# Performance work log

Measured on AMD Instinct MI355X. Metric: run time of the kernel, lower is better.

Reference implementation:

```python
import jax, jax.numpy as jnp
import numpy as np

B, N, F_IN, H, E = 8, 10000, 128, 128, 160000


def setup_inputs() -> dict:
    key = jax.random.key(0)
    ks = jax.random.split(key, 6)
    x = jax.random.normal(ks[0], (B, N, F_IN), dtype=jnp.float32)
    edge_index = jax.random.randint(ks[1], (2, E), 0, N, dtype=jnp.int64)
    # GCNConv params (glorot-ish scale), LayerNorm affine params
    W1 = jax.random.normal(ks[2], (F_IN, H), dtype=jnp.float32) / np.sqrt(F_IN)
    b1 = jnp.zeros((H,), dtype=jnp.float32)
    W2 = jax.random.normal(ks[3], (H, H), dtype=jnp.float32) / np.sqrt(H)
    b2 = jnp.zeros((H,), dtype=jnp.float32)
    ln_w = jnp.ones((H,), dtype=jnp.float32)
    ln_b = jnp.zeros((H,), dtype=jnp.float32)
    return {"x": x, "edge_index": edge_index, "W1": W1, "b1": b1,
            "W2": W2, "b2": b2, "ln_w": ln_w, "ln_b": ln_b}


def reference(x, edge_index, W1, b1, W2, b2, ln_w, ln_b):
    # x: [B, N, F]; edge_index: [2, E] shared across batch (tiled per graph
    # in the original via node offsets -> equivalent to vmapping over batch).
    n = x.shape[1]
    loops = jnp.arange(n, dtype=edge_index.dtype)
    src = jnp.concatenate([edge_index[0], loops])  # add self-loops (GCNConv default)
    dst = jnp.concatenate([edge_index[1], loops])
    # symmetric degree normalization: deg over targets with self-loops
    deg = jax.ops.segment_sum(jnp.ones(dst.shape[0], dtype=x.dtype), dst, num_segments=n)
    dinv = jnp.where(deg > 0, jax.lax.rsqrt(deg), 0.0)
    w_e = dinv[src] * dinv[dst]  # [E+N] per-edge norm

    def gcn_agg(h):  # h: [B, N, H] -> gather, scale, scatter-add
        msg = h[:, src, :] * w_e[None, :, None]  # [B, E+N, H]
        return jax.vmap(lambda m: jax.ops.segment_sum(m, dst, num_segments=n))(msg)

    h1 = jax.nn.relu(gcn_agg(x @ W1) + b1)
    h2 = gcn_agg(h1 @ W2) + b2
    # LayerNorm over last dim (eps=1e-5, torch default)
    mu = jnp.mean(h2, axis=-1, keepdims=True)
    var = jnp.mean(jnp.square(h2 - mu), axis=-1, keepdims=True)
    out = (h2 - mu) * jax.lax.rsqrt(var + 1e-5) * ln_w + ln_b
    return out  # [B, N, H]
```

## Files before the change

kernel.cpp:

```cpp
#include <hip/hip_runtime.h>
#include <hip/hip_bf16.h>

#define NNODES 10000
#define NB 8
#define NF 128
#define NE 160000

typedef __attribute__((ext_vector_type(8))) short  short8;
typedef __attribute__((ext_vector_type(8))) unsigned short ushort8;
typedef __attribute__((ext_vector_type(4))) float  f32x4;

__device__ __forceinline__ unsigned short f2b(float f) {
    union { float f; unsigned u; } v; v.f = f;
    unsigned r = v.u + 0x7FFF + ((v.u >> 16) & 1);
    return (unsigned short)(r >> 16);
}
__device__ __forceinline__ float b2f(unsigned short h) {
    union { unsigned u; float f; } v; v.u = ((unsigned)h) << 16;
    return v.f;
}
__device__ __forceinline__ float b2f_lo(unsigned u) {
    union { unsigned u; float f; } v; v.u = u << 16; return v.f;
}
__device__ __forceinline__ float b2f_hi(unsigned u) {
    union { unsigned u; float f; } v; v.u = u & 0xffff0000u; return v.f;
}


__global__ void k_zero(int* __restrict__ cnt, int* __restrict__ fill) {
    int i = blockIdx.x * blockDim.x + threadIdx.x;
    if (i < NNODES) { cnt[i] = 0; fill[i] = 0; }
}

__global__ void k_count(const int* __restrict__ ei, int* __restrict__ cnt) {
    int e = blockIdx.x * blockDim.x + threadIdx.x;
    if (e < NE) atomicAdd(&cnt[ei[NE + e]], 1);
}

__global__ void k_dinv(const int* __restrict__ cnt, float* __restrict__ dinv) {
    int i = blockIdx.x * blockDim.x + threadIdx.x;
    if (i < NNODES) dinv[i] = rsqrtf((float)(cnt[i] + 1));
}

__global__ void k_scan(const int* __restrict__ cnt, int* __restrict__ row_ptr) {
    __shared__ int part[1024];
    int t = threadIdx.x;
    const int CH = (NNODES + 1023) / 1024;
    int lo = t * CH, hi = min(lo + CH, NNODES);
    int s = 0;
    for (int i = lo; i < hi; i++) s += cnt[i];
    part[t] = s;
    __syncthreads();
    for (int off = 1; off < 1024; off <<= 1) {
        int v = (t >= off) ? part[t - off] : 0;
        __syncthreads();
        part[t] += v;
        __syncthreads();
    }
    int base = part[t] - s;
    for (int i = lo; i < hi; i++) { row_ptr[i] = base; base += cnt[i]; }
    if (t == 1023) row_ptr[NNODES] = part[1023];
}

__global__ void k_scatter(const int* __restrict__ ei, const int* __restrict__ row_ptr,
                          int* __restrict__ fill, const float* __restrict__ dinv,
                          int* __restrict__ col, float* __restrict__ wgt) {
    int e = blockIdx.x * blockDim.x + threadIdx.x;
    if (e >= NE) return;
    int s = ei[e];
    int d = ei[NE + e];
    int pos = row_ptr[d] + atomicAdd(&fill[d], 1);
    col[pos] = s;
    wgt[pos] = dinv[s] * dinv[d];
}

__global__ void k_wt(const float* __restrict__ W, unsigned short* __restrict__ Wt) {
    int id = blockIdx.x * 256 + threadIdx.x;
    int n = id >> 7, k = id & 127;
    Wt[(size_t)n * 128 + k] = f2b(W[(size_t)k * 128 + n]);
}

template <bool ABF16>
__global__ __launch_bounds__(256) void k_mm_mfma(const void* __restrict__ Ap,
                                                 const unsigned short* __restrict__ Wt,
                                                 unsigned short* __restrict__ Cn) {
    __shared__ unsigned short wlds[128 * 136];
    const int t = threadIdx.x;
    {
        const int r = t >> 1, h = t & 1;
        const ushort8* src = (const ushort8*)(Wt + r * 128 + h * 64);
        #pragma unroll
        for (int i = 0; i < 8; i++)
            *(ushort8*)(wlds + r * 136 + h * 64 + i * 8) = src[i];
    }
    __syncthreads();

    const int wid = t >> 6, lane = t & 63;
    const int quad = lane >> 4, l16 = lane & 15;
    const int m0 = blockIdx.x * 64 + (wid & 1) * 32;
    const int nb = (wid >> 1) * 64;
    const int kq = quad * 8;

    f32x4 acc[2][4] = {};

    #pragma unroll
    for (int ks = 0; ks < 128; ks += 32) {
        short8 bf[2];
        #pragma unroll
        for (int mi = 0; mi < 2; mi++) {
            const size_t row = (size_t)(m0 + mi * 16 + l16);
            if constexpr (ABF16) {
                bf[mi] = *(const short8*)((const unsigned short*)Ap + row * 128 + ks + kq);
            } else {
                const float* p = (const float*)Ap + row * 128 + ks + kq;
                float4 u0 = *(const float4*)p;
                float4 u1 = *(const float4*)(p + 4);
                short8 v;
                v[0] = (short)f2b(u0.x); v[1] = (short)f2b(u0.y);
                v[2] = (short)f2b(u0.z); v[3] = (short)f2b(u0.w);
                v[4] = (short)f2b(u1.x); v[5] = (short)f2b(u1.y);
                v[6] = (short)f2b(u1.z); v[7] = (short)f2b(u1.w);
                bf[mi] = v;
            }
        }
        short8 af[4];
        #pragma unroll
        for (int ni = 0; ni < 4; ni++)
            af[ni] = *(const short8*)(wlds + (nb + ni * 16 + l16) * 136 + ks + kq);
        #pragma unroll
        for (int mi = 0; mi < 2; mi++)
            #pragma unroll
            for (int ni = 0; ni < 4; ni++)
                acc[mi][ni] = __builtin_amdgcn_mfma_f32_16x16x32_bf16(
                    af[ni], bf[mi], acc[mi][ni], 0, 0, 0);
    }

    __syncthreads();
    {
        const int rbase = (wid & 1) * 32;
        #pragma unroll
        for (int mi = 0; mi < 2; mi++) {
            int rr = rbase + mi * 16 + l16;
            #pragma unroll
            for (int ni = 0; ni < 4; ni++) {
                ushort4 o;
                o.x = f2b(acc[mi][ni][0]); o.y = f2b(acc[mi][ni][1]);
                o.z = f2b(acc[mi][ni][2]); o.w = f2b(acc[mi][ni][3]);
                *(ushort4*)(wlds + rr * 136 + nb + ni * 16 + quad * 4) = o;
            }
        }
    }
    __syncthreads();
    {
        const int r = t >> 2, seg = t & 3;
        int gm = blockIdx.x * 64 + r;
        int b = gm / NNODES;
        int n = gm - b * NNODES;
        unsigned short* dst = Cn + ((size_t)n * NB + b) * 128 + seg * 32;
        const unsigned short* srow = wlds + r * 136 + seg * 32;
        #pragma unroll
        for (int i = 0; i < 4; i++)
            *(ushort8*)(dst + i * 8) = *(const ushort8*)(srow + i * 8);
    }
}


__global__ __launch_bounds__(256) void k_agg_relu(const unsigned int* __restrict__ hNu,
                                                  const float* __restrict__ bias,
                                                  const int* __restrict__ row_ptr,
                                                  const int* __restrict__ col,
                                                  const float* __restrict__ wgt,
                                                  const float* __restrict__ dinv,
                                                  unsigned int* __restrict__ h1u) {
    const int t = threadIdx.x;
    const int b = blockIdx.x & 7;
    const int g = blockIdx.x >> 3;
    const int wid = __builtin_amdgcn_readfirstlane(t >> 6);
    const int lane = t & 63;
    const int n = g * 4 + wid;

    const unsigned int* base = hNu + (size_t)b * 64 + lane;
    float di = dinv[n];
    float wself = di * di;
    unsigned int u = base[(size_t)n * 512];
    float a0 = b2f_lo(u) * wself;
    float a1 = b2f_hi(u) * wself;

    int e = row_ptr[n], e1 = row_ptr[n + 1];
    for (; e + 4 <= e1; e += 4) {
        int s0 = col[e], s1 = col[e + 1], s2 = col[e + 2], s3 = col[e + 3];
        float w0 = wgt[e], w1 = wgt[e + 1], w2 = wgt[e + 2], w3 = wgt[e + 3];
        unsigned int u0 = base[(size_t)s0 * 512];
        unsigned int u1 = base[(size_t)s1 * 512];
        unsigned int u2 = base[(size_t)s2 * 512];
        unsigned int u3 = base[(size_t)s3 * 512];
        a0 = fmaf(b2f_lo(u0), w0, a0); a1 = fmaf(b2f_hi(u0), w0, a1);
        a0 = fmaf(b2f_lo(u1), w1, a0); a1 = fmaf(b2f_hi(u1), w1, a1);
        a0 = fmaf(b2f_lo(u2), w2, a0); a1 = fmaf(b2f_hi(u2), w2, a1);
        a0 = fmaf(b2f_lo(u3), w3, a0); a1 = fmaf(b2f_hi(u3), w3, a1);
    }
    for (; e < e1; ++e) {
        int s = col[e]; float w = wgt[e];
        unsigned int uu = base[(size_t)s * 512];
        a0 = fmaf(b2f_lo(uu), w, a0); a1 = fmaf(b2f_hi(uu), w, a1);
    }
    a0 = fmaxf(a0 + bias[lane * 2], 0.f);
    a1 = fmaxf(a1 + bias[lane * 2 + 1], 0.f);
    unsigned int o = (unsigned int)f2b(a0) | ((unsigned int)f2b(a1) << 16);
    __builtin_nontemporal_store(o, &h1u[((size_t)b * NNODES + n) * 64 + lane]);
}

__global__ __launch_bounds__(256) void k_agg_ln(const unsigned int* __restrict__ hNu,
                                                const float* __restrict__ bias,
                                                const int* __restrict__ row_ptr,
                                                const int* __restrict__ col,
                                                const float* __restrict__ wgt,
                                                const float* __restrict__ dinv,
                                                const float* __restrict__ ln_w,
                                                const float* __restrict__ ln_b,
                                                float* __restrict__ out) {
    const int t = threadIdx.x;
    const int b = blockIdx.x & 7;
    const int g = blockIdx.x >> 3;
    const int wid = __builtin_amdgcn_readfirstlane(t >> 6);
    const int lane = t & 63;
    const int n = g * 4 + wid;

    const unsigned int* base = hNu + (size_t)b * 64 + lane;
    float di = dinv[n];
    float wself = di * di;
    unsigned int u = base[(size_t)n * 512];
    float a0 = b2f_lo(u) * wself;
    float a1 = b2f_hi(u) * wself;

    int e = row_ptr[n], e1 = row_ptr[n + 1];
    for (; e + 4 <= e1; e += 4) {
        int s0 = col[e], s1 = col[e + 1], s2 = col[e + 2], s3 = col[e + 3];
        float w0 = wgt[e], w1 = wgt[e + 1], w2 = wgt[e + 2], w3 = wgt[e + 3];
        unsigned int u0 = base[(size_t)s0 * 512];
        unsigned int u1 = base[(size_t)s1 * 512];
        unsigned int u2 = base[(size_t)s2 * 512];
        unsigned int u3 = base[(size_t)s3 * 512];
        a0 = fmaf(b2f_lo(u0), w0, a0); a1 = fmaf(b2f_hi(u0), w0, a1);
        a0 = fmaf(b2f_lo(u1), w1, a0); a1 = fmaf(b2f_hi(u1), w1, a1);
        a0 = fmaf(b2f_lo(u2), w2, a0); a1 = fmaf(b2f_hi(u2), w2, a1);
        a0 = fmaf(b2f_lo(u3), w3, a0); a1 = fmaf(b2f_hi(u3), w3, a1);
    }
    for (; e < e1; ++e) {
        int s = col[e]; float w = wgt[e];
        unsigned int uu = base[(size_t)s * 512];
        a0 = fmaf(b2f_lo(uu), w, a0); a1 = fmaf(b2f_hi(uu), w, a1);
    }
    a0 += bias[lane * 2];
    a1 += bias[lane * 2 + 1];

    float s1 = a0 + a1;
    float s2 = a0 * a0 + a1 * a1;
    #pragma unroll
    for (int m = 1; m < 64; m <<= 1) {
        s1 += __shfl_xor(s1, m);
        s2 += __shfl_xor(s2, m);
    }
    float mu = s1 * (1.f / NF);
    float var = s2 * (1.f / NF) - mu * mu;
    float rs = rsqrtf(var + 1e-5f);

    float o0 = (a0 - mu) * rs * ln_w[lane * 2] + ln_b[lane * 2];
    float o1 = (a1 - mu) * rs * ln_w[lane * 2 + 1] + ln_b[lane * 2 + 1];
    float* dst = out + ((size_t)b * NNODES + n) * 128 + lane * 2;
    __builtin_nontemporal_store(o0, dst);
    __builtin_nontemporal_store(o1, dst + 1);
}


extern "C" void kernel_launch(void* const* d_in, const int* in_sizes, int n_in,
                              void* d_out, int out_size, void* d_ws, size_t ws_size,
                              hipStream_t stream) {
    const float* x    = (const float*)d_in[0];
    const int*   ei   = (const int*)d_in[1];
    const float* W1   = (const float*)d_in[2];
    const float* b1   = (const float*)d_in[3];
    const float* W2   = (const float*)d_in[4];
    const float* b2   = (const float*)d_in[5];
    const float* ln_w = (const float*)d_in[6];
    const float* ln_b = (const float*)d_in[7];
    float* out = (float*)d_out;

    char* ws = (char*)d_ws;
    int*            cnt     = (int*)(ws + 0);
    int*            fill    = (int*)(ws + 40192);
    int*            row_ptr = (int*)(ws + 80384);
    float*          dinv    = (float*)(ws + 120832);
    int*            col     = (int*)(ws + 161024);
    float*          wgt     = (float*)(ws + 801024);
    unsigned short* hA16    = (unsigned short*)(ws + 1441024);
    unsigned short* h1b     = (unsigned short*)(ws + 21921024);
    unsigned short* Wt1     = (unsigned short*)cnt;
    unsigned short* Wt2     = (unsigned short*)fill;

    k_zero   <<<(NNODES + 255) / 256, 256, 0, stream>>>(cnt, fill);
    k_count  <<<(NE + 255) / 256, 256, 0, stream>>>(ei, cnt);
    k_dinv   <<<(NNODES + 255) / 256, 256, 0, stream>>>(cnt, dinv);
    k_scan   <<<1, 1024, 0, stream>>>(cnt, row_ptr);
    k_scatter<<<(NE + 255) / 256, 256, 0, stream>>>(ei, row_ptr, fill, dinv, col, wgt);

    k_wt<<<64, 256, 0, stream>>>(W1, Wt1);
    k_wt<<<64, 256, 0, stream>>>(W2, Wt2);

    k_mm_mfma<false><<<(NB * NNODES) / 64, 256, 0, stream>>>(x, Wt1, hA16);
    k_agg_relu<<<(NNODES / 4) * NB, 256, 0, stream>>>((const unsigned int*)hA16, b1,
                                                      row_ptr, col, wgt, dinv,
                                                      (unsigned int*)h1b);

    k_mm_mfma<true><<<(NB * NNODES) / 64, 256, 0, stream>>>(h1b, Wt2, hA16);
    k_agg_ln<<<(NNODES / 4) * NB, 256, 0, stream>>>((const unsigned int*)hA16, b2,
                                                    row_ptr, col, wgt, dinv,
                                                    ln_w, ln_b, out);
}
```

Baseline: 240.0 us.

## Pack edges into uint2, fuse setup kernels, enlarge GEMM tiles, deepen gather unroll

Interleaves the CSR column index and edge weight into a single uint2 array so each aggregated edge needs one load instead of two. The dinv kernel is folded into the scan, and the two weight transposes share one launch, cutting launch count. The MFMA GEMM now covers 128 rows per block instead of 64, and bf16 conversion uses packed pair conversions. The aggregation loops unroll by 8 to keep more gathers in flight, at the cost of more registers.

```diff
diff --git a/kernel.cpp b/kernel.cpp
--- a/kernel.cpp
+++ b/kernel.cpp
@@ -15,9 +15,10 @@
     unsigned r = v.u + 0x7FFF + ((v.u >> 16) & 1);
     return (unsigned short)(r >> 16);
 }
-__device__ __forceinline__ float b2f(unsigned short h) {
-    union { unsigned u; float f; } v; v.u = ((unsigned)h) << 16;
-    return v.f;
+__device__ __forceinline__ unsigned int f2b2(float a, float b) {
+    union { __hip_bfloat162 h; unsigned int u; } v;
+    v.h = __float22bfloat162_rn(make_float2(a, b));
+    return v.u;
 }
 __device__ __forceinline__ float b2f_lo(unsigned u) {
     union { unsigned u; float f; } v; v.u = u << 16; return v.f;
@@ -29,7 +30,8 @@
 
 __global__ void k_zero(int* __restrict__ cnt, int* __restrict__ fill) {
     int i = blockIdx.x * blockDim.x + threadIdx.x;
-    if (i < NNODES) { cnt[i] = 0; fill[i] = 0; }
+    if (i < NNODES) cnt[i] = 0;
+    else if (i < 2 * NNODES) fill[i - NNODES] = 0;
 }
 
 __global__ void k_count(const int* __restrict__ ei, int* __restrict__ cnt) {
@@ -37,18 +39,18 @@
     if (e < NE) atomicAdd(&cnt[ei[NE + e]], 1);
 }
 
-__global__ void k_dinv(const int* __restrict__ cnt, float* __restrict__ dinv) {
-    int i = blockIdx.x * blockDim.x + threadIdx.x;
-    if (i < NNODES) dinv[i] = rsqrtf((float)(cnt[i] + 1));
-}
-
-__global__ void k_scan(const int* __restrict__ cnt, int* __restrict__ row_ptr) {
+__global__ void k_scan(const int* __restrict__ cnt, int* __restrict__ row_ptr,
+                       float* __restrict__ dinv) {
     __shared__ int part[1024];
     int t = threadIdx.x;
     const int CH = (NNODES + 1023) / 1024;
     int lo = t * CH, hi = min(lo + CH, NNODES);
     int s = 0;
-    for (int i = lo; i < hi; i++) s += cnt[i];
+    for (int i = lo; i < hi; i++) {
+        int c = cnt[i];
+        dinv[i] = rsqrtf((float)(c + 1));
+        s += c;
+    }
     part[t] = s;
     __syncthreads();
     for (int off = 1; off < 1024; off <<= 1) {
@@ -64,18 +66,21 @@
 
 __global__ void k_scatter(const int* __restrict__ ei, const int* __restrict__ row_ptr,
                           int* __restrict__ fill, const float* __restrict__ dinv,
-                          int* __restrict__ col, float* __restrict__ wgt) {
+                          uint2* __restrict__ edge) {
     int e = blockIdx.x * blockDim.x + threadIdx.x;
     if (e >= NE) return;
     int s = ei[e];
     int d = ei[NE + e];
     int pos = row_ptr[d] + atomicAdd(&fill[d], 1);
-    col[pos] = s;
-    wgt[pos] = dinv[s] * dinv[d];
-}
-
-__global__ void k_wt(const float* __restrict__ W, unsigned short* __restrict__ Wt) {
-    int id = blockIdx.x * 256 + threadIdx.x;
+    edge[pos] = make_uint2((unsigned)s, __float_as_uint(dinv[s] * dinv[d]));
+}
+
+__global__ void k_wt2(const float* __restrict__ W1, unsigned short* __restrict__ Wt1,
+                      const float* __restrict__ W2, unsigned short* __restrict__ Wt2) {
+    int bid = blockIdx.x;
+    const float* W = (bid < 64) ? W1 : W2;
+    unsigned short* Wt = (bid < 64) ? Wt1 : Wt2;
+    int id = (bid & 63) * 256 + threadIdx.x;
     int n = id >> 7, k = id & 127;
     Wt[(size_t)n * 128 + k] = f2b(W[(size_t)k * 128 + n]);
 }
@@ -97,17 +102,17 @@
 
     const int wid = t >> 6, lane = t & 63;
     const int quad = lane >> 4, l16 = lane & 15;
-    const int m0 = blockIdx.x * 64 + (wid & 1) * 32;
+    const int m0 = blockIdx.x * 128 + (wid & 1) * 64;
     const int nb = (wid >> 1) * 64;
     const int kq = quad * 8;
 
-    f32x4 acc[2][4] = {};
+    f32x4 acc[4][4] = {};
 
     #pragma unroll
     for (int ks = 0; ks < 128; ks += 32) {
-        short8 bf[2];
-        #pragma unroll
-        for (int mi = 0; mi < 2; mi++) {
+        short8 bf[4];
+        #pragma unroll
+        for (int mi = 0; mi < 4; mi++) {
             const size_t row = (size_t)(m0 + mi * 16 + l16);
             if constexpr (ABF16) {
                 bf[mi] = *(const short8*)((const unsigned short*)Ap + row * 128 + ks + kq);
@@ -115,12 +120,10 @@
                 const float* p = (const float*)Ap + row * 128 + ks + kq;
                 float4 u0 = *(const float4*)p;
                 float4 u1 = *(const float4*)(p + 4);
-                short8 v;
-                v[0] = (short)f2b(u0.x); v[1] = (short)f2b(u0.y);
-                v[2] = (short)f2b(u0.z); v[3] = (short)f2b(u0.w);
-                v[4] = (short)f2b(u1.x); v[5] = (short)f2b(u1.y);
-                v[6] = (short)f2b(u1.z); v[7] = (short)f2b(u1.w);
-                bf[mi] = v;
+                union { uint4 u4; short8 s8; } cv;
+                cv.u4.x = f2b2(u0.x, u0.y); cv.u4.y = f2b2(u0.z, u0.w);
+                cv.u4.z = f2b2(u1.x, u1.y); cv.u4.w = f2b2(u1.z, u1.w);
+                bf[mi] = cv.s8;
             }
         }
         short8 af[4];
@@ -128,7 +131,7 @@
         for (int ni = 0; ni < 4; ni++)
             af[ni] = *(const short8*)(wlds + (nb + ni * 16 + l16) * 136 + ks + kq);
         #pragma unroll
-        for (int mi = 0; mi < 2; mi++)
+        for (int mi = 0; mi < 4; mi++)
             #pragma unroll
             for (int ni = 0; ni < 4; ni++)
                 acc[mi][ni] = __builtin_amdgcn_mfma_f32_16x16x32_bf16(
@@ -137,29 +140,29 @@
 
     __syncthreads();
     {
-        const int rbase = (wid & 1) * 32;
-        #pragma unroll
-        for (int mi = 0; mi < 2; mi++) {
+        const int rbase = (wid & 1) * 64;
+        #pragma unroll
+        for (int mi = 0; mi < 4; mi++) {
             int rr = rbase + mi * 16 + l16;
             #pragma unroll
             for (int ni = 0; ni < 4; ni++) {
-                ushort4 o;
-                o.x = f2b(acc[mi][ni][0]); o.y = f2b(acc[mi][ni][1]);
-                o.z = f2b(acc[mi][ni][2]); o.w = f2b(acc[mi][ni][3]);
-                *(ushort4*)(wlds + rr * 136 + nb + ni * 16 + quad * 4) = o;
+                uint2 p;
+                p.x = f2b2(acc[mi][ni][0], acc[mi][ni][1]);
+                p.y = f2b2(acc[mi][ni][2], acc[mi][ni][3]);
+                *(uint2*)(wlds + rr * 136 + nb + ni * 16 + quad * 4) = p;
             }
         }
     }
     __syncthreads();
     {
-        const int r = t >> 2, seg = t & 3;
-        int gm = blockIdx.x * 64 + r;
+        const int r = t >> 1, h = t & 1;
+        int gm = blockIdx.x * 128 + r;
         int b = gm / NNODES;
         int n = gm - b * NNODES;
-        unsigned short* dst = Cn + ((size_t)n * NB + b) * 128 + seg * 32;
-        const unsigned short* srow = wlds + r * 136 + seg * 32;
-        #pragma unroll
-        for (int i = 0; i < 4; i++)
+        unsigned short* dst = Cn + ((size_t)n * NB + b) * 128 + h * 64;
+        const unsigned short* srow = wlds + r * 136 + h * 64;
+        #pragma unroll
+        for (int i = 0; i < 8; i++)
             *(ushort8*)(dst + i * 8) = *(const ushort8*)(srow + i * 8);
     }
 }
@@ -168,8 +171,7 @@
 __global__ __launch_bounds__(256) void k_agg_relu(const unsigned int* __restrict__ hNu,
                                                   const float* __restrict__ bias,
                                                   const int* __restrict__ row_ptr,
-                                                  const int* __restrict__ col,
-                                                  const float* __restrict__ wgt,
+                                                  const uint2* __restrict__ edge,
                                                   const float* __restrict__ dinv,
                                                   unsigned int* __restrict__ h1u) {
     const int t = threadIdx.x;
@@ -187,34 +189,50 @@
     float a1 = b2f_hi(u) * wself;
 
     int e = row_ptr[n], e1 = row_ptr[n + 1];
+    for (; e + 8 <= e1; e += 8) {
+        uint2 E[8];
+        #pragma unroll
+        for (int j = 0; j < 8; j++) E[j] = edge[e + j];
+        unsigned int U[8];
+        #pragma unroll
+        for (int j = 0; j < 8; j++) U[j] = base[(size_t)E[j].x * 512];
+        #pragma unroll
+        for (int j = 0; j < 8; j++) {
+            float w = __uint_as_float(E[j].y);
+            a0 = fmaf(b2f_lo(U[j]), w, a0);
+            a1 = fmaf(b2f_hi(U[j]), w, a1);
+        }
+    }
     for (; e + 4 <= e1; e += 4) {
-        int s0 = col[e], s1 = col[e + 1], s2 = col[e + 2], s3 = col[e + 3];
-        float w0 = wgt[e], w1 = wgt[e + 1], w2 = wgt[e + 2], w3 = wgt[e + 3];
-        unsigned int u0 = base[(size_t)s0 * 512];
-        unsigned int u1 = base[(size_t)s1 * 512];
-        unsigned int u2 = base[(size_t)s2 * 512];
-        unsigned int u3 = base[(size_t)s3 * 512];
-        a0 = fmaf(b2f_lo(u0), w0, a0); a1 = fmaf(b2f_hi(u0), w0, a1);
-        a0 = fmaf(b2f_lo(u1), w1, a0); a1 = fmaf(b2f_hi(u1), w1, a1);
-        a0 = fmaf(b2f_lo(u2), w2, a0); a1 = fmaf(b2f_hi(u2), w2, a1);
-        a0 = fmaf(b2f_lo(u3), w3, a0); a1 = fmaf(b2f_hi(u3), w3, a1);
+        uint2 E[4];
+        #pragma unroll
+        for (int j = 0; j < 4; j++) E[j] = edge[e + j];
+        unsigned int U[4];
+        #pragma unroll
+        for (int j = 0; j < 4; j++) U[j] = base[(size_t)E[j].x * 512];
+        #pragma unroll
+        for (int j = 0; j < 4; j++) {
+            float w = __uint_as_float(E[j].y);
+            a0 = fmaf(b2f_lo(U[j]), w, a0);
+            a1 = fmaf(b2f_hi(U[j]), w, a1);
+        }
     }
     for (; e < e1; ++e) {
-        int s = col[e]; float w = wgt[e];
-        unsigned int uu = base[(size_t)s * 512];
-        a0 = fmaf(b2f_lo(uu), w, a0); a1 = fmaf(b2f_hi(uu), w, a1);
+        uint2 E = edge[e];
+        float w = __uint_as_float(E.y);
+        unsigned int uu = base[(size_t)E.x * 512];
+        a0 = fmaf(b2f_lo(uu), w, a0);
+        a1 = fmaf(b2f_hi(uu), w, a1);
     }
     a0 = fmaxf(a0 + bias[lane * 2], 0.f);
     a1 = fmaxf(a1 + bias[lane * 2 + 1], 0.f);
-    unsigned int o = (unsigned int)f2b(a0) | ((unsigned int)f2b(a1) << 16);
-    __builtin_nontemporal_store(o, &h1u[((size_t)b * NNODES + n) * 64 + lane]);
+    __builtin_nontemporal_store(f2b2(a0, a1), &h1u[((size_t)b * NNODES + n) * 64 + lane]);
 }
 
 __global__ __launch_bounds__(256) void k_agg_ln(const unsigned int* __restrict__ hNu,
                                                 const float* __restrict__ bias,
                                                 const int* __restrict__ row_ptr,
-                                                const int* __restrict__ col,
-                                                const float* __restrict__ wgt,
+                                                const uint2* __restrict__ edge,
                                                 const float* __restrict__ dinv,
                                                 const float* __restrict__ ln_w,
                                                 const float* __restrict__ ln_b,
@@ -234,22 +252,40 @@
     float a1 = b2f_hi(u) * wself;
 
     int e = row_ptr[n], e1 = row_ptr[n + 1];
+    for (; e + 8 <= e1; e += 8) {
+        uint2 E[8];
+        #pragma unroll
+        for (int j = 0; j < 8; j++) E[j] = edge[e + j];
+        unsigned int U[8];
+        #pragma unroll
+        for (int j = 0; j < 8; j++) U[j] = base[(size_t)E[j].x * 512];
+        #pragma unroll
+        for (int j = 0; j < 8; j++) {
+            float w = __uint_as_float(E[j].y);
+            a0 = fmaf(b2f_lo(U[j]), w, a0);
+            a1 = fmaf(b2f_hi(U[j]), w, a1);
+        }
+    }
     for (; e + 4 <= e1; e += 4) {
-        int s0 = col[e], s1 = col[e + 1], s2 = col[e + 2], s3 = col[e + 3];
-        float w0 = wgt[e], w1 = wgt[e + 1], w2 = wgt[e + 2], w3 = wgt[e + 3];
-        unsigned int u0 = base[(size_t)s0 * 512];
-        unsigned int u1 = base[(size_t)s1 * 512];
-        unsigned int u2 = base[(size_t)s2 * 512];
-        unsigned int u3 = base[(size_t)s3 * 512];
-        a0 = fmaf(b2f_lo(u0), w0, a0); a1 = fmaf(b2f_hi(u0), w0, a1);
-        a0 = fmaf(b2f_lo(u1), w1, a0); a1 = fmaf(b2f_hi(u1), w1, a1);
-        a0 = fmaf(b2f_lo(u2), w2, a0); a1 = fmaf(b2f_hi(u2), w2, a1);
-        a0 = fmaf(b2f_lo(u3), w3, a0); a1 = fmaf(b2f_hi(u3), w3, a1);
+        uint2 E[4];
+        #pragma unroll
+        for (int j = 0; j < 4; j++) E[j] = edge[e + j];
+        unsigned int U[4];
+        #pragma unroll
+        for (int j = 0; j < 4; j++) U[j] = base[(size_t)E[j].x * 512];
+        #pragma unroll
+        for (int j = 0; j < 4; j++) {
+            float w = __uint_as_float(E[j].y);
+            a0 = fmaf(b2f_lo(U[j]), w, a0);
+            a1 = fmaf(b2f_hi(U[j]), w, a1);
+        }
     }
     for (; e < e1; ++e) {
-        int s = col[e]; float w = wgt[e];
-        unsigned int uu = base[(size_t)s * 512];
-        a0 = fmaf(b2f_lo(uu), w, a0); a1 = fmaf(b2f_hi(uu), w, a1);
+        uint2 E = edge[e];
+        float w = __uint_as_float(E.y);
+        unsigned int uu = base[(size_t)E.x * 512];
+        a0 = fmaf(b2f_lo(uu), w, a0);
+        a1 = fmaf(b2f_hi(uu), w, a1);
     }
     a0 += bias[lane * 2];
     a1 += bias[lane * 2 + 1];
@@ -291,29 +327,25 @@
     int*            fill    = (int*)(ws + 40192);
     int*            row_ptr = (int*)(ws + 80384);
     float*          dinv    = (float*)(ws + 120832);
-    int*            col     = (int*)(ws + 161024);
-    float*          wgt     = (float*)(ws + 801024);
+    uint2*          edge    = (uint2*)(ws + 161024);
     unsigned short* hA16    = (unsigned short*)(ws + 1441024);
     unsigned short* h1b     = (unsigned short*)(ws + 21921024);
     unsigned short* Wt1     = (unsigned short*)cnt;
     unsigned short* Wt2     = (unsigned short*)fill;
 
-    k_zero   <<<(NNODES + 255) / 256, 256, 0, stream>>>(cnt, fill);
+    k_zero   <<<(2 * NNODES + 255) / 256, 256, 0, stream>>>(cnt, fill);
     k_count  <<<(NE + 255) / 256, 256, 0, stream>>>(ei, cnt);
-    k_dinv   <<<(NNODES + 255) / 256, 256, 0, stream>>>(cnt, dinv);
-    k_scan   <<<1, 1024, 0, stream>>>(cnt, row_ptr);
-    k_scatter<<<(NE + 255) / 256, 256, 0, stream>>>(ei, row_ptr, fill, dinv, col, wgt);
-
-    k_wt<<<64, 256, 0, stream>>>(W1, Wt1);
-    k_wt<<<64, 256, 0, stream>>>(W2, Wt2);
-
-    k_mm_mfma<false><<<(NB * NNODES) / 64, 256, 0, stream>>>(x, Wt1, hA16);
+    k_scan   <<<1, 1024, 0, stream>>>(cnt, row_ptr, dinv);
+    k_scatter<<<(NE + 255) / 256, 256, 0, stream>>>(ei, row_ptr, fill, dinv, edge);
+    k_wt2    <<<128, 256, 0, stream>>>(W1, Wt1, W2, Wt2);
+
+    k_mm_mfma<false><<<(NB * NNODES) / 128, 256, 0, stream>>>(x, Wt1, hA16);
     k_agg_relu<<<(NNODES / 4) * NB, 256, 0, stream>>>((const unsigned int*)hA16, b1,
-                                                      row_ptr, col, wgt, dinv,
+                                                      row_ptr, edge, dinv,
                                                       (unsigned int*)h1b);
 
-    k_mm_mfma<true><<<(NB * NNODES) / 64, 256, 0, stream>>>(h1b, Wt2, hA16);
+    k_mm_mfma<true><<<(NB * NNODES) / 128, 256, 0, stream>>>(h1b, Wt2, hA16);
     k_agg_ln<<<(NNODES / 4) * NB, 256, 0, stream>>>((const unsigned int*)hA16, b2,
-                                                    row_ptr, col, wgt, dinv,
+                                                    row_ptr, edge, dinv,
                                                     ln_w, ln_b, out);
 }
```

After: 231.6 us. 3.5% less time.
